# Performance work log

Hardware: AMD Instinct MI355X
Metric: run time of the kernel (lower is better)

## Reference

```python
import jax, jax.numpy as jnp
import numpy as np

D_MODEL = 512
NHEAD = 8
SEQ = 2048
BATCH = 4


def setup_inputs() -> dict:
    key = jax.random.key(0)
    ks = jax.random.split(key, 6)
    s = 0.02
    return {
        "x": jax.random.normal(ks[0], (SEQ, BATCH, D_MODEL), jnp.float32),
        "w_in_g": jax.random.normal(ks[1], (3 * D_MODEL, D_MODEL), jnp.float32) * s,
        "b_in_g": jnp.zeros((3 * D_MODEL,), jnp.float32),
        "w_out_g": jax.random.normal(ks[2], (D_MODEL, D_MODEL), jnp.float32) * s,
        "b_out_g": jnp.zeros((D_MODEL,), jnp.float32),
        "w_in_l": jax.random.normal(ks[3], (3 * D_MODEL, D_MODEL), jnp.float32) * s,
        "b_in_l": jnp.zeros((3 * D_MODEL,), jnp.float32),
        "w_out_l": jax.random.normal(ks[4], (D_MODEL, D_MODEL), jnp.float32) * s,
        "b_out_l": jnp.zeros((D_MODEL,), jnp.float32),
        "local_window_size": 128,
    }


def _mha(x, w_in, b_in, w_out, b_out, nhead):
    # x: (S, B, D); faithful to torch nn.MultiheadAttention (batch_first=False)
    S, B, D = x.shape
    dh = D // nhead
    qkv = x @ w_in.T + b_in                       # (S, B, 3D)
    q, k, v = jnp.split(qkv, 3, axis=-1)
    q = q.reshape(S, B, nhead, dh)
    k = k.reshape(S, B, nhead, dh)
    v = v.reshape(S, B, nhead, dh)
    scores = jnp.einsum("sbhd,tbhd->bhst", q, k) / jnp.sqrt(jnp.float32(dh))
    attn = jax.nn.softmax(scores, axis=-1)        # (B, H, S, S)
    out = jnp.einsum("bhst,tbhd->sbhd", attn, v).reshape(S, B, D)
    return out @ w_out.T + b_out


def reference(x, w_in_g, b_in_g, w_out_g, b_out_g,
              w_in_l, b_in_l, w_out_l, b_out_l, local_window_size):
    S, B, D = x.shape
    W = int(local_window_size)
    global_out = _mha(x, w_in_g, b_in_g, w_out_g, b_out_g, NHEAD)
    # Non-overlapping local windows tile the sequence (S % W == 0 here),
    # so the per-window loop == window-batched attention.
    nW = S // W
    xw = x.reshape(nW, W, B, D).transpose(1, 0, 2, 3).reshape(W, nW * B, D)
    lw = _mha(xw, w_in_l, b_in_l, w_out_l, b_out_l, NHEAD)
    local_out = lw.reshape(W, nW, B, D).transpose(1, 0, 2, 3).reshape(S, B, D)
    return global_out + local_out
```

## Files before the change

### kernel.cpp

```cpp
#include <hip/hip_runtime.h>
#include <hip/hip_bf16.h>
#include <stdint.h>

typedef __attribute__((ext_vector_type(8))) short bf16x8;
typedef __attribute__((ext_vector_type(8))) unsigned short u16x8;
typedef __attribute__((ext_vector_type(4))) float f32x4;

#define DEV __device__ __forceinline__

DEV f32x4 mfma16(bf16x8 a, bf16x8 b, f32x4 c) {
  return __builtin_amdgcn_mfma_f32_16x16x32_bf16(a, b, c, 0, 0, 0);
}

DEV void gload_lds16(const void* g, void* l) {
  __builtin_amdgcn_global_load_lds(
      (__attribute__((address_space(1))) void*)(g),
      (__attribute__((address_space(3))) void*)(l), 16, 0, 0);
}

DEV unsigned short f2bf(float f) {
  __hip_bfloat16 h = __float2bfloat16(f);
  return __builtin_bit_cast(unsigned short, h);
}

__global__ __launch_bounds__(256) void convert_all(
    const float4* __restrict__ s0, const float4* __restrict__ s1,
    const float4* __restrict__ s2, const float4* __restrict__ s3,
    const float4* __restrict__ s4, ushort4* __restrict__ dst)
{
  const int n0 = 1048576, n1 = 196608, n3 = 65536;
  int i = blockIdx.x * 256 + threadIdx.x;
  const float4* s; int off;
  if (i < n0)                 { s = s0; off = 0; }
  else if (i < n0 + n1)       { s = s1; off = n0; }
  else if (i < n0 + 2*n1)     { s = s2; off = n0 + n1; }
  else if (i < n0 + 2*n1+n3)  { s = s3; off = n0 + 2*n1; }
  else                        { s = s4; off = n0 + 2*n1 + n3; }
  float4 v = s[i - off];
  ushort4 o;
  o.x = f2bf(v.x); o.y = f2bf(v.y); o.z = f2bf(v.z); o.w = f2bf(v.w);
  dst[i] = o;
}

#define GEMM_STAGE(Ap, Wp, k0v, bufi)                                          \
  {                                                                            \
    _Pragma("unroll")                                                          \
    for (int is = 0; is < 2; ++is) {                                           \
      const int row = is*64 + (t >> 3);                                        \
      const int slot = (t & 7) ^ (row & 7);                                    \
      gload_lds16((Ap) + (long)(m0 + row)*K + (k0v) + slot*8,                  \
                  (char*)&As[bufi][0] + (is*512 + t)*16);                      \
      gload_lds16((Wp) + (long)(n0 + row)*K + (k0v) + slot*8,                  \
                  (char*)&Ws[bufi][0] + (is*512 + t)*16);                      \
    }                                                                          \
  }

#define GEMM_COMPUTE(cur)                                                      \
  {                                                                            \
    const char* Apl = (const char*)&As[cur][0];                                \
    const char* Wpl = (const char*)&Ws[cur][0];                                \
    __builtin_amdgcn_s_setprio(1);                                             \
    _Pragma("unroll")                                                          \
    for (int kk = 0; kk < 2; ++kk) {                                           \
      bf16x8 af[4], wf[2];                                                     \
      _Pragma("unroll")                                                        \
      for (int i = 0; i < 4; ++i) {                                            \
        const int row = wr*64 + i*16 + l16;                                    \
        const int slot = (kk*4 + g16) ^ (row & 7);                             \
        af[i] = *(const bf16x8*)(Apl + row*128 + slot*16);                     \
      }                                                                        \
      _Pragma("unroll")                                                        \
      for (int j = 0; j < 2; ++j) {                                            \
        const int row = wc*32 + j*16 + l16;                                    \
        const int slot = (kk*4 + g16) ^ (row & 7);                             \
        wf[j] = *(const bf16x8*)(Wpl + row*128 + slot*16);                     \
      }                                                                        \
      _Pragma("unroll")                                                        \
      for (int i = 0; i < 4; ++i)                                              \
        _Pragma("unroll")                                                      \
        for (int j = 0; j < 2; ++j)                                            \
          acc[i][j] = mfma16(af[i], wf[j], acc[i][j]);                         \
    }                                                                          \
    __builtin_amdgcn_s_setprio(0);                                             \
  }

__global__ __launch_bounds__(512) void gemm_qkv(
    const __hip_bfloat16* __restrict__ A0, const __hip_bfloat16* __restrict__ W0,
    const float* __restrict__ b0,
    __hip_bfloat16* __restrict__ qkp, __hip_bfloat16* __restrict__ vtp,
    int M, int N, int K)
{
  __shared__ __attribute__((aligned(16))) char SMEM[65536];
  __hip_bfloat16 (*As)[8192] = (__hip_bfloat16(*)[8192])SMEM;
  __hip_bfloat16 (*Ws)[8192] = (__hip_bfloat16(*)[8192])(SMEM + 32768);
  const int t = threadIdx.x;
  const int lane = t & 63, wid = t >> 6;
  const int g16 = lane >> 4, l16 = lane & 15;
  const int wr = wid >> 2, wc = wid & 3;
  const int lid = blockIdx.x + (blockIdx.y << 6);
  const int xcd = lid & 7, pos = lid >> 3;
  const int m0 = (xcd*8 + (pos & 7)) * 128, n0 = (pos >> 3) * 128;

  f32x4 acc[4][2] = {};
  const int nks = K >> 6;

  GEMM_STAGE(A0, W0, 0, 0)
  for (int step = 0; step < nks; ++step) {
    const int cur = step & 1;
    if (step + 1 < nks) {
      GEMM_STAGE(A0, W0, (step+1) << 6, cur ^ 1)
      asm volatile("s_waitcnt vmcnt(4)" ::: "memory");
    } else {
      asm volatile("s_waitcnt vmcnt(0)" ::: "memory");
    }
    __builtin_amdgcn_s_barrier();
    asm volatile("" ::: "memory");
    GEMM_COMPUTE(cur)
    asm volatile("" ::: "memory");
    __builtin_amdgcn_s_barrier();
  }

  if (n0 < 1024) {
#pragma unroll
    for (int i = 0; i < 4; ++i) {
      const int gr = m0 + wr*64 + i*16 + g16*4;
#pragma unroll
      for (int j = 0; j < 2; ++j) {
        const int gc = n0 + wc*32 + j*16 + l16;
        const float bias = b0[gc];
        const float scl = (gc >= 512) ? 0.180336880f : 1.0f;
#pragma unroll
        for (int r = 0; r < 4; ++r)
          qkp[(long)(gr + r)*1024 + gc] =
              __float2bfloat16((acc[i][j][r] + bias) * scl);
      }
    }
  } else {
    const int n0l = n0 - 1024;
    short* T = (short*)SMEM;
#pragma unroll
    for (int i = 0; i < 4; ++i) {
      const int sl = wr*16 + i*4 + g16;
#pragma unroll
      for (int j = 0; j < 2; ++j) {
        const int gcl = wc*32 + j*16 + l16;
        const float bias = b0[n0 + gcl];
#pragma unroll
        for (int r = 0; r < 4; ++r)
          T[gcl*136 + r*32 + sl] = (short)f2bf(acc[i][j][r] + bias);
      }
    }
    __syncthreads();
    const int d = t & 127, b4 = t >> 7;
    __hip_bfloat16* dst = vtp + ((long)(b4*512 + n0l + d))*2048 + (m0 >> 2);
#pragma unroll
    for (int k = 0; k < 4; ++k) {
      u16x8 v = *(const u16x8*)(T + d*136 + b4*32 + k*8);
      *(u16x8*)(dst + k*8) = v;
    }
  }
}

__global__ __launch_bounds__(512) void gemm_out(
    const __hip_bfloat16* __restrict__ A0, const __hip_bfloat16* __restrict__ W0,
    const float* __restrict__ b0,
    const __hip_bfloat16* __restrict__ A1, const __hip_bfloat16* __restrict__ W1,
    const float* __restrict__ b1,
    float* __restrict__ Cout, int M, int N, int K)
{
  __shared__ __attribute__((aligned(16))) __hip_bfloat16 As[2][128*64];
  __shared__ __attribute__((aligned(16))) __hip_bfloat16 Ws[2][128*64];
  const int t = threadIdx.x;
  const int lane = t & 63, wid = t >> 6;
  const int g16 = lane >> 4, l16 = lane & 15;
  const int wr = wid >> 2, wc = wid & 3;
  const int lid = blockIdx.x + (blockIdx.y << 6);
  const int xcd = lid & 7, pos = lid >> 3;
  const int m0 = (xcd*8 + (pos & 7)) * 128, n0 = (pos >> 3) * 128;

  f32x4 acc[4][2] = {};
  const int nks = K >> 6;
  const int NS = 2*nks;

  GEMM_STAGE(A0, W0, 0, 0)
  for (int step = 0; step < NS; ++step) {
    const int cur = step & 1;
    if (step + 1 < NS) {
      const int nstep = step + 1;
      const __hip_bfloat16* Ap = (nstep >= nks) ? A1 : A0;
      const __hip_bfloat16* Wp = (nstep >= nks) ? W1 : W0;
      const int k0 = ((nstep >= nks) ? (nstep - nks) : nstep) << 6;
      GEMM_STAGE(Ap, Wp, k0, cur ^ 1)
      asm volatile("s_waitcnt vmcnt(4)" ::: "memory");
    } else {
      asm volatile("s_waitcnt vmcnt(0)" ::: "memory");
    }
    __builtin_amdgcn_s_barrier();
    asm volatile("" ::: "memory");
    GEMM_COMPUTE(cur)
    asm volatile("" ::: "memory");
    __builtin_amdgcn_s_barrier();
  }

#pragma unroll
  for (int i = 0; i < 4; ++i) {
    const int gr = m0 + wr*64 + i*16 + g16*4;
#pragma unroll
    for (int j = 0; j < 2; ++j) {
      const int gc = n0 + wc*32 + j*16 + l16;
      const float bias = b0[gc] + b1[gc];
#pragma unroll
      for (int r = 0; r < 4; ++r)
        Cout[(long)(gr + r)*N + gc] = acc[i][j][r] + bias;
    }
  }
}

__global__ __launch_bounds__(512) void flash_all(
    const __hip_bfloat16* __restrict__ qkg, const __hip_bfloat16* __restrict__ vtg,
    __hip_bfloat16* __restrict__ outg,
    const __hip_bfloat16* __restrict__ qkl, const __hip_bfloat16* __restrict__ vtl,
    __hip_bfloat16* __restrict__ outl,
    const int* __restrict__ wptr, int S, int B, int blkoff)
{
  const int t = threadIdx.x, lane = t & 63, w = t >> 6;
  const int g16 = lane >> 4, l16 = lane & 15;
  const int gid = blockIdx.x + blkoff;
  const int isl = gid >= 512;
  const int id = gid & 511;
  const __hip_bfloat16* qk = isl ? qkl : qkg;
  const __hip_bfloat16* vt = isl ? vtl : vtg;
  __hip_bfloat16* outb = isl ? outl : outg;
  const int Wn = isl ? wptr[0] : S;
  const int xcd = id & 7, seq = id >> 3;
  const int bh = xcd + 8*(seq & 3);
  const int qt = seq >> 2;
  const int b = bh >> 3, h = bh & 7;
  const int q0 = qt * 128;
  const int kv0 = (q0 / Wn) * Wn;
  const int nkt = Wn >> 6;
  const int vtb = bh * 64;

  __shared__ __attribute__((aligned(16))) __hip_bfloat16 Kb[2][64*64];
  __shared__ __attribute__((aligned(16))) __hip_bfloat16 Vb[2][64*64];
  __shared__ __attribute__((aligned(16))) short Pl[8][16*72];

  const int qrow = q0 + w*16 + l16;
  bf16x8 qa[2];
  {
    const __hip_bfloat16* qp = qk + ((long)qrow*B + b)*1024 + h*64 + g16*8;
    qa[0] = *(const bf16x8*)(const void*)qp;
    qa[1] = *(const bf16x8*)(const void*)(qp + 32);
  }
  bf16x8 aones;
#pragma unroll
  for (int e = 0; e < 8; ++e) aones[e] = (short)0x3F80;

  f32x4 o[4] = {};
  f32x4 ol = {};

#define STAGE(tile, bufi)                                                      \
  {                                                                            \
    const int kvs_ = kv0 + (tile)*64;                                          \
    const int row_ = t >> 3;                                                   \
    const int sl_ = (t & 7) ^ (row_ & 7);                                      \
    gload_lds16(qk + ((long)(kvs_+row_)*B + b)*1024 + 512 + h*64 + sl_*8,      \
                (char*)&Kb[bufi][0] + t*16);                                   \
    gload_lds16(vt + (long)(vtb + row_)*2048 + kvs_ + sl_*8,                   \
                (char*)&Vb[bufi][0] + t*16);                                   \
  }

  STAGE(0, 0)

  for (int kt = 0; kt < nkt; ++kt) {
    const int cur = kt & 1;
    if (kt + 1 < nkt) {
      STAGE(kt + 1, cur ^ 1)
      asm volatile("s_waitcnt vmcnt(2)" ::: "memory");
    } else {
      asm volatile("s_waitcnt vmcnt(0)" ::: "memory");
    }
    __builtin_amdgcn_s_barrier();
    asm volatile("" ::: "memory");

    f32x4 s[4] = {};
    const char* Kp = (const char*)&Kb[cur][0];
    __builtin_amdgcn_s_setprio(1);
#pragma unroll
    for (int kk = 0; kk < 2; ++kk)
#pragma unroll
      for (int j = 0; j < 4; ++j) {
        const int row = j*16 + l16;
        const int slot = (kk*4 + g16) ^ (row & 7);
        bf16x8 kf = *(const bf16x8*)(Kp + row*128 + slot*16);
        s[j] = mfma16(kf, qa[kk], s[j]);
      }
    __builtin_amdgcn_s_setprio(0);

    short* Pw = &Pl[w][0];
#pragma unroll
    for (int j = 0; j < 4; ++j) {
      short4 pk4;
      pk4.x = (short)f2bf(__builtin_amdgcn_exp2f(s[j][0]));
      pk4.y = (short)f2bf(__builtin_amdgcn_exp2f(s[j][1]));
      pk4.z = (short)f2bf(__builtin_amdgcn_exp2f(s[j][2]));
      pk4.w = (short)f2bf(__builtin_amdgcn_exp2f(s[j][3]));
      *(short4*)(Pw + l16*72 + j*16 + g16*4) = pk4;
    }

    __builtin_amdgcn_s_setprio(1);
#pragma unroll
    for (int kk = 0; kk < 2; ++kk) {
      bf16x8 pf = *(const bf16x8*)(Pw + l16*72 + kk*32 + g16*8);
      ol = mfma16(aones, pf, ol);
#pragma unroll
      for (int dblk = 0; dblk < 4; ++dblk) {
        const int row = dblk*16 + l16;
        const int slot = (kk*4 + g16) ^ (row & 7);
        bf16x8 vf = *(const bf16x8*)((const char*)&Vb[cur][0] + row*128 + slot*16);
        o[dblk] = mfma16(vf, pf, o[dblk]);
      }
    }
    __builtin_amdgcn_s_setprio(0);

    asm volatile("" ::: "memory");
    __builtin_amdgcn_s_barrier();
  }

  const float inv = 1.f / ol[0];
  const long obase = ((long)qrow*B + b)*512 + h*64;
#pragma unroll
  for (int dblk = 0; dblk < 4; ++dblk) {
    ushort4 pk;
    pk.x = f2bf(o[dblk][0]*inv); pk.y = f2bf(o[dblk][1]*inv);
    pk.z = f2bf(o[dblk][2]*inv); pk.w = f2bf(o[dblk][3]*inv);
    *(ushort4*)(outb + obase + dblk*16 + g16*4) = pk;
  }
}

extern "C" void kernel_launch(void* const* d_in, const int* in_sizes, int n_in,
                              void* d_out, int out_size, void* d_ws, size_t ws_size,
                              hipStream_t stream) {
  const float* x   = (const float*)d_in[0];
  const float* wig = (const float*)d_in[1];
  const float* big = (const float*)d_in[2];
  const float* wog = (const float*)d_in[3];
  const float* bog = (const float*)d_in[4];
  const float* wil = (const float*)d_in[5];
  const float* bil = (const float*)d_in[6];
  const float* wol = (const float*)d_in[7];
  const float* bol = (const float*)d_in[8];
  const int*   wsz = (const int*)d_in[9];

  char* ws = (char*)d_ws;
  __hip_bfloat16* xb    = (__hip_bfloat16*)(ws + 0);
  __hip_bfloat16* wigb  = (__hip_bfloat16*)(ws + 8388608);
  __hip_bfloat16* wilb  = (__hip_bfloat16*)(ws + 9961472);
  __hip_bfloat16* wogb  = (__hip_bfloat16*)(ws + 11534336);
  __hip_bfloat16* wolb  = (__hip_bfloat16*)(ws + 12058624);
  __hip_bfloat16* qkg   = (__hip_bfloat16*)(ws + 12582912);
  __hip_bfloat16* qkl   = (__hip_bfloat16*)(ws + 29360128);
  __hip_bfloat16* vtg   = (__hip_bfloat16*)(ws + 46137344);
  __hip_bfloat16* vtl   = (__hip_bfloat16*)(ws + 54525952);
  __hip_bfloat16* attng = xb;

  const int big_ws = ws_size >= (size_t)71303168;
  __hip_bfloat16* attnl = big_ws ? (__hip_bfloat16*)(ws + 62914560)
                                 : qkg;

  convert_all<<<6144, 256, 0, stream>>>(
      (const float4*)x, (const float4*)wig, (const float4*)wil,
      (const float4*)wog, (const float4*)wol, (ushort4*)ws);

  dim3 gq(64, 12);
  gemm_qkv<<<gq, 512, 0, stream>>>(xb, wigb, big, qkg, vtg, 8192, 1536, 512);
  gemm_qkv<<<gq, 512, 0, stream>>>(xb, wilb, bil, qkl, vtl, 8192, 1536, 512);

  if (big_ws) {
    flash_all<<<1024, 512, 0, stream>>>(qkg, vtg, attng, qkl, vtl, attnl,
                                        wsz, 2048, 4, 0);
  } else {
    flash_all<<<512, 512, 0, stream>>>(qkg, vtg, attng, qkl, vtl, attnl,
                                       wsz, 2048, 4, 0);
    flash_all<<<512, 512, 0, stream>>>(qkg, vtg, attng, qkl, vtl, attnl,
                                       wsz, 2048, 4, 512);
  }

  dim3 go(64, 4);
  gemm_out<<<go, 512, 0, stream>>>(attng, wogb, bog, attnl, wolb, bol,
                                   (float*)d_out, 8192, 512, 512);
}
```

Before: 120.3 us.

## Split global attention KV range in halves and combine partial results

Global attention blocks now each cover half of the key/value sequence, doubling the number of global blocks so the GPU has more work units to balance against the short local-window blocks. Each half writes unnormalized bf16 outputs and row sums, and a new combine kernel adds them and normalizes. The split reuses the output buffer and the weight workspace as scratch. It relies on a fixed softmax offset with no running max, so halves combine by plain addition. The cost is an extra kernel launch, extra memory traffic, and bf16 rounding of the unnormalized partial sums.

```diff
diff --git a/kernel.cpp b/kernel.cpp
--- a/kernel.cpp
+++ b/kernel.cpp
@@ -21,6 +21,10 @@
 DEV unsigned short f2bf(float f) {
   __hip_bfloat16 h = __float2bfloat16(f);
   return __builtin_bit_cast(unsigned short, h);
+}
+
+DEV float bf2f(unsigned short u) {
+  return __builtin_bit_cast(float, (unsigned)u << 16);
 }
 
 __global__ __launch_bounds__(256) void convert_all(
@@ -218,27 +222,28 @@
 
 __global__ __launch_bounds__(512) void flash_all(
     const __hip_bfloat16* __restrict__ qkg, const __hip_bfloat16* __restrict__ vtg,
-    __hip_bfloat16* __restrict__ outg,
     const __hip_bfloat16* __restrict__ qkl, const __hip_bfloat16* __restrict__ vtl,
+    __hip_bfloat16* __restrict__ oa, __hip_bfloat16* __restrict__ ob,
+    float* __restrict__ la, float* __restrict__ lb,
     __hip_bfloat16* __restrict__ outl,
     const int* __restrict__ wptr, int S, int B, int blkoff)
 {
   const int t = threadIdx.x, lane = t & 63, w = t >> 6;
   const int g16 = lane >> 4, l16 = lane & 15;
   const int gid = blockIdx.x + blkoff;
-  const int isl = gid >= 512;
-  const int id = gid & 511;
+  const int isl = gid >= 1024;
+  const int half = isl ? 0 : (gid >> 9);
+  const int id = isl ? (gid - 1024) : (gid & 511);
   const __hip_bfloat16* qk = isl ? qkl : qkg;
   const __hip_bfloat16* vt = isl ? vtl : vtg;
-  __hip_bfloat16* outb = isl ? outl : outg;
-  const int Wn = isl ? wptr[0] : S;
   const int xcd = id & 7, seq = id >> 3;
   const int bh = xcd + 8*(seq & 3);
   const int qt = seq >> 2;
   const int b = bh >> 3, h = bh & 7;
   const int q0 = qt * 128;
-  const int kv0 = (q0 / Wn) * Wn;
-  const int nkt = Wn >> 6;
+  int kv0, nkt;
+  if (isl) { const int Wn = wptr[0]; kv0 = (q0 / Wn) * Wn; nkt = Wn >> 6; }
+  else     { kv0 = half * (S >> 1);  nkt = S >> 7; }
   const int vtb = bh * 64;
 
   __shared__ __attribute__((aligned(16))) __hip_bfloat16 Kb[2][64*64];
@@ -327,15 +332,46 @@
     __builtin_amdgcn_s_barrier();
   }
 
-  const float inv = 1.f / ol[0];
   const long obase = ((long)qrow*B + b)*512 + h*64;
-#pragma unroll
-  for (int dblk = 0; dblk < 4; ++dblk) {
-    ushort4 pk;
-    pk.x = f2bf(o[dblk][0]*inv); pk.y = f2bf(o[dblk][1]*inv);
-    pk.z = f2bf(o[dblk][2]*inv); pk.w = f2bf(o[dblk][3]*inv);
-    *(ushort4*)(outb + obase + dblk*16 + g16*4) = pk;
-  }
+  if (isl) {
+    const float inv = 1.f / ol[0];
+#pragma unroll
+    for (int dblk = 0; dblk < 4; ++dblk) {
+      ushort4 pk;
+      pk.x = f2bf(o[dblk][0]*inv); pk.y = f2bf(o[dblk][1]*inv);
+      pk.z = f2bf(o[dblk][2]*inv); pk.w = f2bf(o[dblk][3]*inv);
+      *(ushort4*)(outl + obase + dblk*16 + g16*4) = pk;
+    }
+  } else {
+    __hip_bfloat16* op = half ? ob : oa;
+#pragma unroll
+    for (int dblk = 0; dblk < 4; ++dblk) {
+      ushort4 pk;
+      pk.x = f2bf(o[dblk][0]); pk.y = f2bf(o[dblk][1]);
+      pk.z = f2bf(o[dblk][2]); pk.w = f2bf(o[dblk][3]);
+      *(ushort4*)(op + obase + dblk*16 + g16*4) = pk;
+    }
+    if (g16 == 0)
+      (half ? lb : la)[((long)qrow*B + b)*8 + h] = ol[0];
+  }
+}
+
+__global__ __launch_bounds__(256) void combine_halves(
+    const __hip_bfloat16* __restrict__ oa, const __hip_bfloat16* __restrict__ ob,
+    const float* __restrict__ la, const float* __restrict__ lb,
+    __hip_bfloat16* __restrict__ outg)
+{
+  const int i = blockIdx.x*256 + threadIdx.x;
+  const int row = i >> 6, c0 = (i & 63) << 3;
+  const int h = c0 >> 6;
+  const float inv = 1.f / (la[(long)row*8 + h] + lb[(long)row*8 + h]);
+  u16x8 a = *(const u16x8*)(oa + (long)row*512 + c0);
+  u16x8 bb = *(const u16x8*)(ob + (long)row*512 + c0);
+  u16x8 r;
+#pragma unroll
+  for (int e = 0; e < 8; ++e)
+    r[e] = f2bf((bf2f(a[e]) + bf2f(bb[e])) * inv);
+  *(u16x8*)(outg + (long)row*512 + c0) = r;
 }
 
 extern "C" void kernel_launch(void* const* d_in, const int* in_sizes, int n_in,
@@ -362,6 +398,11 @@
   __hip_bfloat16* qkl   = (__hip_bfloat16*)(ws + 29360128);
   __hip_bfloat16* vtg   = (__hip_bfloat16*)(ws + 46137344);
   __hip_bfloat16* vtl   = (__hip_bfloat16*)(ws + 54525952);
+
+  __hip_bfloat16* oa    = xb;
+  __hip_bfloat16* ob    = (__hip_bfloat16*)d_out;
+  float*          la    = (float*)(ws + 8388608);
+  float*          lb    = (float*)(ws + 8650752);
   __hip_bfloat16* attng = xb;
 
   const int big_ws = ws_size >= (size_t)71303168;
@@ -377,14 +418,16 @@
   gemm_qkv<<<gq, 512, 0, stream>>>(xb, wilb, bil, qkl, vtl, 8192, 1536, 512);
 
   if (big_ws) {
-    flash_all<<<1024, 512, 0, stream>>>(qkg, vtg, attng, qkl, vtl, attnl,
-                                        wsz, 2048, 4, 0);
+    flash_all<<<1536, 512, 0, stream>>>(qkg, vtg, qkl, vtl, oa, ob, la, lb,
+                                        attnl, wsz, 2048, 4, 0);
   } else {
-    flash_all<<<512, 512, 0, stream>>>(qkg, vtg, attng, qkl, vtl, attnl,
-                                       wsz, 2048, 4, 0);
-    flash_all<<<512, 512, 0, stream>>>(qkg, vtg, attng, qkl, vtl, attnl,
-                                       wsz, 2048, 4, 512);
-  }
+    flash_all<<<1024, 512, 0, stream>>>(qkg, vtg, qkl, vtl, oa, ob, la, lb,
+                                        attnl, wsz, 2048, 4, 0);
+    flash_all<<<512, 512, 0, stream>>>(qkg, vtg, qkl, vtl, oa, ob, la, lb,
+                                       attnl, wsz, 2048, 4, 1024);
+  }
+
+  combine_halves<<<2048, 256, 0, stream>>>(oa, ob, la, lb, attng);
 
   dim3 go(64, 4);
   gemm_out<<<go, 512, 0, stream>>>(attng, wogb, bog, attnl, wolb, bol,
```

New measurement: 127.2 us. 1.06x slower.
